# Kernel optimization log

Measured on AMD Instinct MI355X. Metric: run time of the kernel, lower is better.

## Reference

```python
import jax, jax.numpy as jnp
import numpy as np

N_NODES = 100000
N_EDGES = 1600000
NFEAT, NHID, NCLASS = 128, 64, 40


def setup_inputs() -> dict:
    key = jax.random.key(0)
    k = jax.random.split(key, 6)
    x = jax.random.normal(k[0], (N_NODES, NFEAT), dtype=jnp.float32)
    edge_index = jax.random.randint(k[1], (2, N_EDGES), 0, N_NODES, dtype=jnp.int64)
    edge_weight = jax.random.uniform(k[2], (N_EDGES,), dtype=jnp.float32)
    # Glorot-style init as in PyG GCNConv.reset_parameters
    W1 = jax.random.normal(k[3], (NFEAT, NHID), dtype=jnp.float32) * (1.0 / np.sqrt(NFEAT))
    b1 = jnp.zeros((NHID,), dtype=jnp.float32)
    W2 = jax.random.normal(k[4], (NHID, NCLASS), dtype=jnp.float32) * (1.0 / np.sqrt(NHID))
    b2 = jnp.zeros((NCLASS,), dtype=jnp.float32)
    return {"x": x, "edge_index": edge_index, "edge_weight": edge_weight,
            "W1": W1, "b1": b1, "W2": W2, "b2": b2}


def _gcn_conv(x, edge_index, edge_weight, W, b):
    """PyG GCNConv: add self-loops, symmetric gcn_norm, linear, scatter-add, bias."""
    n = x.shape[0]
    loop = jnp.arange(n)
    row = jnp.concatenate([edge_index[0], loop])  # source nodes
    col = jnp.concatenate([edge_index[1], loop])  # target nodes
    w = jnp.concatenate([edge_weight, jnp.ones((n,), edge_weight.dtype)])
    deg = jax.ops.segment_sum(w, col, num_segments=n)          # [N]
    dinv = jnp.where(deg > 0, jax.lax.rsqrt(deg), 0.0)
    norm = dinv[row] * w * dinv[col]                           # [E+N]
    h = x @ W                                                  # [N, out]
    msg = norm[:, None] * h[row]                               # gather: [E+N, out]
    out = jax.ops.segment_sum(msg, col, num_segments=n)        # scatter-add: [N, out]
    return out + b


def reference(x, edge_index, edge_weight, W1, b1, W2, b2):
    h = jax.nn.relu(_gcn_conv(x, edge_index, edge_weight, W1, b1))
    # F.dropout with training=False is identity (eval mode)
    return _gcn_conv(h, edge_index, edge_weight, W2, b2)
```

## Files before the change

kernel.cpp:

```cpp
#include <hip/hip_runtime.h>
#include <hip/hip_bf16.h>

#define N_NODES 100000
#define N_EDGES 1600000
#define NFEAT 128
#define NHID 64
#define NCLASS 40
#define CAP 64

#define BIN_SHIFT 9
#define BIN_NODES 512
#define NBIN ((N_NODES + BIN_NODES - 1) / BIN_NODES)
#define SCAP 10240
#define CHUNK 2048
#define LCAP 32


__device__ __forceinline__ unsigned pack2(float a, float b) {
    unsigned ua = __float_as_uint(a), ub = __float_as_uint(b);
    unsigned ra = (ua + 0x7FFFu + ((ua >> 16) & 1u)) >> 16;
    unsigned rb = (ub + 0x7FFFu + ((ub >> 16) & 1u)) >> 16;
    return ra | (rb << 16);
}
__device__ __forceinline__ float lo16(unsigned w) { return __uint_as_float(w << 16); }
__device__ __forceinline__ float hi16(unsigned w) { return __uint_as_float(w & 0xFFFF0000u); }


__global__ __launch_bounds__(256) void bin_kernel(const int* __restrict__ ei,
                                                  const float* __restrict__ ew,
                                                  int* __restrict__ bincnt,
                                                  uint2* __restrict__ staging) {
    __shared__ int lcnt[NBIN];
    __shared__ int gbase[NBIN];
    __shared__ int scanbuf[256];
    __shared__ int totals;
    __shared__ uint2 lbuf[NBIN * LCAP];
    int t = threadIdx.x;
    for (int i = t; i < NBIN; i += 256) lcnt[i] = 0;
    __syncthreads();

    int base = blockIdx.x * CHUNK;
#pragma unroll
    for (int u = 0; u < CHUNK / 256; ++u) {
        int e = base + u * 256 + t;
        if (e < N_EDGES) {
            int c = ei[N_EDGES + e];
            int r = ei[e];
            float w = ew[e];
            unsigned wq = (unsigned)fminf(w * 32768.0f, 32767.0f);
            uint2 en = make_uint2(((unsigned)r << 15) | wq, (unsigned)c);
            int b = c >> BIN_SHIFT;
            int p = atomicAdd(&lcnt[b], 1);
            if (p < LCAP) {
                lbuf[b * LCAP + p] = en;
            } else {
                int g = atomicAdd(&bincnt[b], 1);
                if (g < SCAP) staging[(size_t)b * SCAP + g] = en;
            }
        }
    }
    __syncthreads();

    int clamped = (t < NBIN) ? min(lcnt[t], LCAP) : 0;
    if (t < NBIN) gbase[t] = (clamped > 0) ? atomicAdd(&bincnt[t], clamped) : 0;
    scanbuf[t] = clamped;
    __syncthreads();
    for (int o = 1; o < 256; o <<= 1) {
        int add = (t >= o) ? scanbuf[t - o] : 0;
        __syncthreads();
        scanbuf[t] += add;
        __syncthreads();
    }
    if (t < NBIN) lcnt[t] = scanbuf[t] - clamped;
    if (t == NBIN - 1) totals = scanbuf[t];
    __syncthreads();

    int total = totals;
    for (int i = t; i < total; i += 256) {
        int lo = 0, hi = NBIN - 1;
#pragma unroll
        for (int s = 0; s < 8; ++s) {
            int mid = (lo + hi + 1) >> 1;
            if (lcnt[mid] <= i) lo = mid; else hi = mid - 1;
        }
        int idx = i - lcnt[lo];
        int gp = gbase[lo] + idx;
        if (gp < SCAP) staging[(size_t)lo * SCAP + gp] = lbuf[lo * LCAP + idx];
    }
}


__global__ __launch_bounds__(256) void place_kernel(const int* __restrict__ bincnt,
                                                    const uint2* __restrict__ staging,
                                                    unsigned* __restrict__ bucket,
                                                    int* __restrict__ cnt,
                                                    float* __restrict__ dinv) {
    __shared__ int lpos[BIN_NODES];
    __shared__ float lws[BIN_NODES];
    int b = blockIdx.x;
    int t = threadIdx.x;
    for (int i = t; i < BIN_NODES; i += 256) { lpos[i] = 0; lws[i] = 0.0f; }
    __syncthreads();

    int nodebase = b << BIN_SHIFT;
    int n = bincnt[b];
    if (n > SCAP) n = SCAP;
    const uint2* st = staging + (size_t)b * SCAP;
    for (int i = t; i < n; i += 256) {
        uint2 en = st[i];
        int local = (int)en.y - nodebase;
        int p = atomicAdd(&lpos[local], 1);
        if (p < CAP) bucket[((size_t)en.y << 6) + p] = en.x;
        atomicAdd(&lws[local], (float)(en.x & 32767u) * (1.0f / 32768.0f));
    }
    __syncthreads();
    for (int i = t; i < BIN_NODES; i += 256) {
        int node = nodebase + i;
        if (node < N_NODES) {
            cnt[node] = min(lpos[i], CAP);
            dinv[node] = rsqrtf(1.0f + lws[i]);
        }
    }
}


__global__ __launch_bounds__(256) void gemm1_kernel(const float* __restrict__ x,
                                                    const float* __restrict__ W1,
                                                    unsigned short* __restrict__ h1b) {
    __shared__ float sB[NFEAT * NHID];
    int t = threadIdx.x;
    const float4* W4 = (const float4*)W1;
    float4* sB4 = (float4*)sB;
#pragma unroll
    for (int i = 0; i < 8; ++i) sB4[t + 256 * i] = W4[t + 256 * i];
    __syncthreads();

    int tx = t & 15;
    int ty = t >> 4;
    int row0 = blockIdx.x * 64 + ty * 4;
    int c0 = tx * 4;

    const float* xr[4];
#pragma unroll
    for (int i = 0; i < 4; ++i) {
        int r = row0 + i;
        if (r > N_NODES - 1) r = N_NODES - 1;
        xr[i] = x + (size_t)r * NFEAT;
    }

    float acc[4][4] = {};

#pragma unroll 2
    for (int k = 0; k < NFEAT; k += 4) {
        float4 a[4];
#pragma unroll
        for (int i = 0; i < 4; ++i) a[i] = *(const float4*)(xr[i] + k);
#pragma unroll
        for (int kk = 0; kk < 4; ++kk) {
            float4 bb = *(const float4*)(sB + (k + kk) * NHID + c0);
#pragma unroll
            for (int i = 0; i < 4; ++i) {
                float av = (kk == 0) ? a[i].x : (kk == 1) ? a[i].y : (kk == 2) ? a[i].z : a[i].w;
                acc[i][0] += av * bb.x;
                acc[i][1] += av * bb.y;
                acc[i][2] += av * bb.z;
                acc[i][3] += av * bb.w;
            }
        }
    }
#pragma unroll
    for (int i = 0; i < 4; ++i) {
        int r = row0 + i;
        if (r < N_NODES) {
            uint2 p = make_uint2(pack2(acc[i][0], acc[i][1]), pack2(acc[i][2], acc[i][3]));
            *(uint2*)(h1b + (size_t)r * NHID + c0) = p;
        }
    }
}


__global__ __launch_bounds__(256) void gather1_kernel(
        const int* __restrict__ cnt, const unsigned* __restrict__ bucket,
        const float* __restrict__ dinv, const unsigned short* __restrict__ h1b,
        const float* __restrict__ b1, float* __restrict__ relu1) {
    int t = threadIdx.x;
    int lane = t & 63;
    int wave = t >> 6;
    int g = lane >> 3;
    int l = lane & 7;
    int node = (blockIdx.x * 4 + wave) * 8 + g;
    bool nvalid = node < N_NODES;
    int nd = nvalid ? node : N_NODES - 1;
    int d = cnt[nd];
    float dc = dinv[nd];

    uint4 eb0 = *(const uint4*)(bucket + ((size_t)nd << 6) + l * 8);
    uint4 eb1 = *(const uint4*)(bucket + ((size_t)nd << 6) + l * 8 + 4);
    int rl[8]; float wl[8];
#pragma unroll
    for (int k = 0; k < 8; ++k) {
        unsigned e = (k < 4) ? ((const unsigned*)&eb0)[k] : ((const unsigned*)&eb1)[k - 4];
        int slot = l * 8 + k;
        bool ok = slot < d;
        int r = ok ? (int)(e >> 15) : 0;
        rl[k] = r;
        wl[k] = ok ? (float)(e & 32767u) * (1.0f / 32768.0f) * dinv[r] : 0.0f;
    }

    uint4 hs = *(const uint4*)(h1b + (size_t)nd * NHID + l * 8);
    float acc[8];
#pragma unroll
    for (int k = 0; k < 4; ++k) {
        unsigned w = ((const unsigned*)&hs)[k];
        acc[2 * k] = dc * lo16(w);
        acc[2 * k + 1] = dc * hi16(w);
    }

    for (int j = 0; j < d; j += 8) {
        int src = (g << 3) + (j >> 3);
        int r[8]; float w[8];
#pragma unroll
        for (int k = 0; k < 8; ++k) { r[k] = __shfl(rl[k], src); w[k] = __shfl(wl[k], src); }
        uint4 v[8];
#pragma unroll
        for (int k = 0; k < 8; ++k)
            v[k] = *(const uint4*)(h1b + (size_t)r[k] * NHID + l * 8);
#pragma unroll
        for (int k = 0; k < 8; ++k) {
#pragma unroll
            for (int q = 0; q < 4; ++q) {
                unsigned ww = ((const unsigned*)&v[k])[q];
                acc[2 * q] += w[k] * lo16(ww);
                acc[2 * q + 1] += w[k] * hi16(ww);
            }
        }
    }
    if (nvalid) {
        float4 bv0 = *(const float4*)(b1 + l * 8);
        float4 bv1 = *(const float4*)(b1 + l * 8 + 4);
        float4 o0 = make_float4(fmaxf(dc * acc[0] + bv0.x, 0.0f), fmaxf(dc * acc[1] + bv0.y, 0.0f),
                                fmaxf(dc * acc[2] + bv0.z, 0.0f), fmaxf(dc * acc[3] + bv0.w, 0.0f));
        float4 o1 = make_float4(fmaxf(dc * acc[4] + bv1.x, 0.0f), fmaxf(dc * acc[5] + bv1.y, 0.0f),
                                fmaxf(dc * acc[6] + bv1.z, 0.0f), fmaxf(dc * acc[7] + bv1.w, 0.0f));
        *(float4*)(relu1 + (size_t)node * NHID + l * 8) = o0;
        *(float4*)(relu1 + (size_t)node * NHID + l * 8 + 4) = o1;
    }
}


__global__ __launch_bounds__(256) void gemm2_kernel(const float* __restrict__ in,
                                                    const float* __restrict__ W2,
                                                    unsigned short* __restrict__ h2b) {
    __shared__ float sB[NHID * NCLASS];
    int t = threadIdx.x;
    for (int i = t; i < NHID * NCLASS; i += 256) sB[i] = W2[i];
    __syncthreads();

    int row = blockIdx.x * 256 + t;
    bool valid = row < N_NODES;
    int r = valid ? row : N_NODES - 1;
    float acc[NCLASS] = {};

#pragma unroll 2
    for (int k = 0; k < NHID; k += 4) {
        float4 a = *(const float4*)(in + (size_t)r * NHID + k);
#pragma unroll
        for (int kk = 0; kk < 4; ++kk) {
            float av = (kk == 0) ? a.x : (kk == 1) ? a.y : (kk == 2) ? a.z : a.w;
#pragma unroll
            for (int cg = 0; cg < 10; ++cg) {
                float4 bb = *(const float4*)(sB + (k + kk) * NCLASS + cg * 4);
                acc[cg * 4 + 0] += av * bb.x;
                acc[cg * 4 + 1] += av * bb.y;
                acc[cg * 4 + 2] += av * bb.z;
                acc[cg * 4 + 3] += av * bb.w;
            }
        }
    }
    if (valid) {
#pragma unroll
        for (int cg = 0; cg < 5; ++cg) {
            uint4 p;
            p.x = pack2(acc[cg * 8 + 0], acc[cg * 8 + 1]);
            p.y = pack2(acc[cg * 8 + 2], acc[cg * 8 + 3]);
            p.z = pack2(acc[cg * 8 + 4], acc[cg * 8 + 5]);
            p.w = pack2(acc[cg * 8 + 6], acc[cg * 8 + 7]);
            *(uint4*)(h2b + (size_t)row * NCLASS + cg * 8) = p;
        }
    }
}


__global__ __launch_bounds__(256) void gather2_kernel(
        const int* __restrict__ cnt, const unsigned* __restrict__ bucket,
        const float* __restrict__ dinv, const unsigned short* __restrict__ h2b,
        const float* __restrict__ b2, float* __restrict__ out) {
    int t = threadIdx.x;
    int lane = t & 63;
    int wave = t >> 6;
    int g = lane >> 4;
    int l = lane & 15;
    int node = (blockIdx.x * 4 + wave) * 4 + g;
    bool nvalid = node < N_NODES;
    int nd = nvalid ? node : N_NODES - 1;
    int d = cnt[nd];
    float dc = dinv[nd];
    bool fvalid = (l < 10);

    uint4 eb = *(const uint4*)(bucket + ((size_t)nd << 6) + l * 4);
    int rl[4]; float wl[4];
#pragma unroll
    for (int k = 0; k < 4; ++k) {
        unsigned e = ((const unsigned*)&eb)[k];
        int slot = l * 4 + k;
        bool ok = slot < d;
        int r = ok ? (int)(e >> 15) : 0;
        rl[k] = r;
        wl[k] = ok ? (float)(e & 32767u) * (1.0f / 32768.0f) * dinv[r] : 0.0f;
    }

    float acc[4] = {};
    int lc = fvalid ? l * 4 : 0;
    if (fvalid) {
        uint2 hs = *(const uint2*)(h2b + (size_t)nd * NCLASS + lc);
        acc[0] = dc * lo16(hs.x); acc[1] = dc * hi16(hs.x);
        acc[2] = dc * lo16(hs.y); acc[3] = dc * hi16(hs.y);
    }

    for (int j = 0; j < d; j += 4) {
        int src = (g << 4) + (j >> 2);
        int r0 = __shfl(rl[0], src), r1 = __shfl(rl[1], src);
        int r2 = __shfl(rl[2], src), r3 = __shfl(rl[3], src);
        float w0 = __shfl(wl[0], src), w1 = __shfl(wl[1], src);
        float w2 = __shfl(wl[2], src), w3 = __shfl(wl[3], src);
        if (fvalid) {
            uint2 v0 = *(const uint2*)(h2b + (size_t)r0 * NCLASS + lc);
            uint2 v1 = *(const uint2*)(h2b + (size_t)r1 * NCLASS + lc);
            uint2 v2 = *(const uint2*)(h2b + (size_t)r2 * NCLASS + lc);
            uint2 v3 = *(const uint2*)(h2b + (size_t)r3 * NCLASS + lc);
            acc[0] += w0 * lo16(v0.x) + w1 * lo16(v1.x) + w2 * lo16(v2.x) + w3 * lo16(v3.x);
            acc[1] += w0 * hi16(v0.x) + w1 * hi16(v1.x) + w2 * hi16(v2.x) + w3 * hi16(v3.x);
            acc[2] += w0 * lo16(v0.y) + w1 * lo16(v1.y) + w2 * lo16(v2.y) + w3 * lo16(v3.y);
            acc[3] += w0 * hi16(v0.y) + w1 * hi16(v1.y) + w2 * hi16(v2.y) + w3 * hi16(v3.y);
        }
    }
    if (nvalid && fvalid) {
        float4 bv = *(const float4*)(b2 + l * 4);
        *(float4*)(out + (size_t)node * NCLASS + l * 4) =
            make_float4(dc * acc[0] + bv.x, dc * acc[1] + bv.y,
                        dc * acc[2] + bv.z, dc * acc[3] + bv.w);
    }
}


extern "C" void kernel_launch(void* const* d_in, const int* in_sizes, int n_in,
                              void* d_out, int out_size, void* d_ws, size_t ws_size,
                              hipStream_t stream) {
    const float* x  = (const float*)d_in[0];
    const int*   ei = (const int*)d_in[1];
    const float* ew = (const float*)d_in[2];
    const float* W1 = (const float*)d_in[3];
    const float* b1 = (const float*)d_in[4];
    const float* W2 = (const float*)d_in[5];
    const float* b2 = (const float*)d_in[6];
    float* out = (float*)d_out;

    int*            bincnt = (int*)d_ws;
    int*            cnt    = bincnt + 256;
    float*          dinv   = (float*)(cnt + 100352);
    unsigned*       bucket = (unsigned*)(dinv + 100352);
    unsigned short* h1b    = (unsigned short*)(bucket + (size_t)N_NODES * CAP);
    float*          relu1  = (float*)(h1b + (size_t)N_NODES * NHID);
    uint2*          staging = (uint2*)relu1;
    unsigned short* h2b    = h1b;

    hipMemsetAsync(bincnt, 0, NBIN * sizeof(int), stream);

    bin_kernel<<<(N_EDGES + CHUNK - 1) / CHUNK, 256, 0, stream>>>(ei, ew, bincnt, staging);
    place_kernel<<<NBIN, 256, 0, stream>>>(bincnt, staging, bucket, cnt, dinv);

    gemm1_kernel<<<(N_NODES + 63) / 64, 256, 0, stream>>>(x, W1, h1b);
    gather1_kernel<<<(N_NODES + 31) / 32, 256, 0, stream>>>(cnt, bucket, dinv, h1b, b1, relu1);

    gemm2_kernel<<<(N_NODES + 255) / 256, 256, 0, stream>>>(relu1, W2, h2b);
    gather2_kernel<<<(N_NODES + 15) / 16, 256, 0, stream>>>(cnt, bucket, dinv, h2b, b2, out);
}
```

Measured before the change: 290.9 us.

## Rewrite first-layer GEMM with bf16 MFMA and swizzled LDS tiles

Replaces the FP32 FMA GEMM for x@W1 with a bf16 MFMA 16x16x32 kernel. x rows are converted to bf16 and W1 is pre-transposed to bf16 by a new small prep kernel, and both are stored in XOR-swizzled shared memory to avoid bank conflicts. The bin kernel's per-bin local buffer capacity (LCAP) is also halved, which cuts its shared memory use. This trades input precision (x and W1 rounded to bf16) for matrix-core throughput, and adds one extra kernel launch.

```diff
diff --git a/kernel.cpp b/kernel.cpp
--- a/kernel.cpp
+++ b/kernel.cpp
@@ -13,7 +13,10 @@
 #define NBIN ((N_NODES + BIN_NODES - 1) / BIN_NODES)
 #define SCAP 10240
 #define CHUNK 2048
-#define LCAP 32
+#define LCAP 16
+
+using frag_ab = __attribute__((ext_vector_type(8))) short;
+using frag_cd = __attribute__((ext_vector_type(4))) float;
 
 
 __device__ __forceinline__ unsigned pack2(float a, float b) {
@@ -21,6 +24,10 @@
     unsigned ra = (ua + 0x7FFFu + ((ua >> 16) & 1u)) >> 16;
     unsigned rb = (ub + 0x7FFFu + ((ub >> 16) & 1u)) >> 16;
     return ra | (rb << 16);
+}
+__device__ __forceinline__ unsigned short bf16rtn(float f) {
+    unsigned u = __float_as_uint(f);
+    return (unsigned short)((u + 0x7FFFu + ((u >> 16) & 1u)) >> 16);
 }
 __device__ __forceinline__ float lo16(unsigned w) { return __uint_as_float(w << 16); }
 __device__ __forceinline__ float hi16(unsigned w) { return __uint_as_float(w & 0xFFFF0000u); }
@@ -124,56 +131,81 @@
 }
 
 
+__global__ __launch_bounds__(256) void w1prep_kernel(const float* __restrict__ W1,
+                                                     unsigned short* __restrict__ w1t) {
+    int idx = blockIdx.x * 256 + threadIdx.x;
+    if (idx < NFEAT * NHID) {
+        int k = idx >> 6, n = idx & 63;
+        w1t[n * NFEAT + k] = bf16rtn(W1[idx]);
+    }
+}
+
+
 __global__ __launch_bounds__(256) void gemm1_kernel(const float* __restrict__ x,
-                                                    const float* __restrict__ W1,
+                                                    const unsigned short* __restrict__ w1t,
                                                     unsigned short* __restrict__ h1b) {
-    __shared__ float sB[NFEAT * NHID];
-    int t = threadIdx.x;
-    const float4* W4 = (const float4*)W1;
-    float4* sB4 = (float4*)sB;
-#pragma unroll
-    for (int i = 0; i < 8; ++i) sB4[t + 256 * i] = W4[t + 256 * i];
-    __syncthreads();
-
-    int tx = t & 15;
-    int ty = t >> 4;
-    int row0 = blockIdx.x * 64 + ty * 4;
-    int c0 = tx * 4;
-
-    const float* xr[4];
-#pragma unroll
-    for (int i = 0; i < 4; ++i) {
-        int r = row0 + i;
-        if (r > N_NODES - 1) r = N_NODES - 1;
-        xr[i] = x + (size_t)r * NFEAT;
-    }
-
-    float acc[4][4] = {};
-
-#pragma unroll 2
-    for (int k = 0; k < NFEAT; k += 4) {
-        float4 a[4];
-#pragma unroll
-        for (int i = 0; i < 4; ++i) a[i] = *(const float4*)(xr[i] + k);
-#pragma unroll
-        for (int kk = 0; kk < 4; ++kk) {
-            float4 bb = *(const float4*)(sB + (k + kk) * NHID + c0);
-#pragma unroll
-            for (int i = 0; i < 4; ++i) {
-                float av = (kk == 0) ? a[i].x : (kk == 1) ? a[i].y : (kk == 2) ? a[i].z : a[i].w;
-                acc[i][0] += av * bb.x;
-                acc[i][1] += av * bb.y;
-                acc[i][2] += av * bb.z;
-                acc[i][3] += av * bb.w;
-            }
-        }
-    }
-#pragma unroll
-    for (int i = 0; i < 4; ++i) {
-        int r = row0 + i;
-        if (r < N_NODES) {
-            uint2 p = make_uint2(pack2(acc[i][0], acc[i][1]), pack2(acc[i][2], acc[i][3]));
-            *(uint2*)(h1b + (size_t)r * NHID + c0) = p;
+    __shared__ unsigned short sm[16384];
+    int t = threadIdx.x;
+    int row0 = blockIdx.x * 64;
+
+#pragma unroll
+    for (int p = 0; p < 4; ++p) {
+        int id = p * 256 + t;
+        int r = id >> 4;
+        int c = id & 15;
+        int gr = row0 + r; if (gr > N_NODES - 1) gr = N_NODES - 1;
+        const float* src = x + (size_t)gr * NFEAT + c * 8;
+        float4 f0 = *(const float4*)src;
+        float4 f1 = *(const float4*)(src + 4);
+        uint4 pk = make_uint4(pack2(f0.x, f0.y), pack2(f0.z, f0.w),
+                              pack2(f1.x, f1.y), pack2(f1.z, f1.w));
+        int cs = c ^ (r & 15);
+        *(uint4*)(&sm[r * 128 + cs * 8]) = pk;
+    }
+    const uint4* wt4 = (const uint4*)w1t;
+#pragma unroll
+    for (int p = 0; p < 4; ++p) {
+        int id = p * 256 + t;
+        int n = id >> 4;
+        int c = id & 15;
+        uint4 v = wt4[id];
+        int cs = c ^ (n & 15);
+        *(uint4*)(&sm[8192 + n * 128 + cs * 8]) = v;
+    }
+    __syncthreads();
+
+    int w = t >> 6, l = t & 63;
+    int li = l & 15, q = l >> 4;
+    int arow = w * 16 + li;
+
+    frag_cd acc0 = {0.f, 0.f, 0.f, 0.f};
+    frag_cd acc1 = {0.f, 0.f, 0.f, 0.f};
+    frag_cd acc2 = {0.f, 0.f, 0.f, 0.f};
+    frag_cd acc3 = {0.f, 0.f, 0.f, 0.f};
+
+#pragma unroll
+    for (int kc = 0; kc < 4; ++kc) {
+        int cc = (kc * 4 + q) ^ li;
+        frag_ab a  = *(const frag_ab*)(&sm[arow * 128 + cc * 8]);
+        frag_ab b0 = *(const frag_ab*)(&sm[8192 + (0 * 16 + li) * 128 + cc * 8]);
+        frag_ab b1 = *(const frag_ab*)(&sm[8192 + (1 * 16 + li) * 128 + cc * 8]);
+        frag_ab b2 = *(const frag_ab*)(&sm[8192 + (2 * 16 + li) * 128 + cc * 8]);
+        frag_ab b3 = *(const frag_ab*)(&sm[8192 + (3 * 16 + li) * 128 + cc * 8]);
+        acc0 = __builtin_amdgcn_mfma_f32_16x16x32_bf16(a, b0, acc0, 0, 0, 0);
+        acc1 = __builtin_amdgcn_mfma_f32_16x16x32_bf16(a, b1, acc1, 0, 0, 0);
+        acc2 = __builtin_amdgcn_mfma_f32_16x16x32_bf16(a, b2, acc2, 0, 0, 0);
+        acc3 = __builtin_amdgcn_mfma_f32_16x16x32_bf16(a, b3, acc3, 0, 0, 0);
+    }
+
+#pragma unroll
+    for (int reg = 0; reg < 4; ++reg) {
+        int rrow = row0 + w * 16 + q * 4 + reg;
+        if (rrow < N_NODES) {
+            unsigned short* dst = h1b + (size_t)rrow * NHID + li;
+            dst[0]  = bf16rtn(acc0[reg]);
+            dst[16] = bf16rtn(acc1[reg]);
+            dst[32] = bf16rtn(acc2[reg]);
+            dst[48] = bf16rtn(acc3[reg]);
         }
     }
 }
@@ -371,15 +403,17 @@
     unsigned*       bucket = (unsigned*)(dinv + 100352);
     unsigned short* h1b    = (unsigned short*)(bucket + (size_t)N_NODES * CAP);
     float*          relu1  = (float*)(h1b + (size_t)N_NODES * NHID);
+    unsigned short* w1t    = (unsigned short*)(relu1 + (size_t)N_NODES * NHID);
     uint2*          staging = (uint2*)relu1;
     unsigned short* h2b    = h1b;
 
     hipMemsetAsync(bincnt, 0, NBIN * sizeof(int), stream);
 
+    w1prep_kernel<<<32, 256, 0, stream>>>(W1, w1t);
     bin_kernel<<<(N_EDGES + CHUNK - 1) / CHUNK, 256, 0, stream>>>(ei, ew, bincnt, staging);
     place_kernel<<<NBIN, 256, 0, stream>>>(bincnt, staging, bucket, cnt, dinv);
 
-    gemm1_kernel<<<(N_NODES + 63) / 64, 256, 0, stream>>>(x, W1, h1b);
+    gemm1_kernel<<<(N_NODES + 63) / 64, 256, 0, stream>>>(x, w1t, h1b);
     gather1_kernel<<<(N_NODES + 31) / 32, 256, 0, stream>>>(cnt, bucket, dinv, h1b, b1, relu1);
 
     gemm2_kernel<<<(N_NODES + 255) / 256, 256, 0, stream>>>(relu1, W2, h2b);
```

Result: faster. 275.4 us (-5.3%).
